# Kernel tuning notes

Measured on AMD Instinct MI355X. Metric: run time of the kernel, lower is better.

## Reference

```python
import jax, jax.numpy as jnp
import numpy as np

HID = 1024
N_HEADS = 16
HEAD_DIM = HID // N_HEADS  # 64
SCALE = float(np.sqrt(HEAD_DIM))  # 8.0
# dba_l1 constants from the source
SCALING = float(np.sqrt(0.72676)) * SCALE
CENTER = SCALE ** 2 * 1.12838


def setup_inputs() -> dict:
    key = jax.random.key(0)
    kq, kk, kv = jax.random.split(key, 3)
    B, LQ, LK = 4, 256, 2048
    return {
        "attention_q": jax.random.normal(kq, (B, LQ, HID), dtype=jnp.float32),
        "attention_k": jax.random.normal(kk, (B, LK, HID), dtype=jnp.float32),
        "attention_v": jax.random.normal(kv, (B, LK, HID), dtype=jnp.float32),
        "attn_diag": jnp.ones((N_HEADS, 1, HEAD_DIM), dtype=jnp.float32),
    }


def _dba_l1_logits(Q, K, attn_diag):
    # Q: [B,H,Lq,D], K: [B,H,Lk,D], attn_diag: [H,1,D]
    # Scan over query positions (mirrors the original per-query loop) to avoid
    # materializing the [B,H,Lq,Lk,D] diff tensor.
    qs = jnp.moveaxis(Q, 2, 0)  # [Lq,B,H,D]

    def step(carry, qi):
        # qi: [B,H,D] -> dist: [B,H,Lk]
        dist = jnp.sum(attn_diag * jnp.abs(K - qi[:, :, None, :]), axis=-1)
        # (dist - CENTER) / (-SCALING) == (CENTER - dist) / SCALING
        return carry, (CENTER - dist) / SCALING

    _, logits = jax.lax.scan(step, None, qs)  # [Lq,B,H,Lk]
    return jnp.moveaxis(logits, 0, 2)  # [B,H,Lq,Lk]


def reference(attention_q, attention_k, attention_v, attn_diag):
    B, Lq, _ = attention_q.shape
    Lk = attention_k.shape[1]
    # split heads: [B,L,hid] -> [B,H,L,D]
    Q = attention_q.reshape(B, Lq, N_HEADS, HEAD_DIM).transpose(0, 2, 1, 3)
    K = attention_k.reshape(B, Lk, N_HEADS, HEAD_DIM).transpose(0, 2, 1, 3)
    V = attention_v.reshape(B, Lk, N_HEADS, HEAD_DIM).transpose(0, 2, 1, 3)

    attn_logits = _dba_l1_logits(Q, K, attn_diag)  # [B,H,Lq,Lk]
    attention = jax.nn.softmax(attn_logits, axis=-1)
    x = jnp.einsum("bhqk,bhkd->bhqd", attention, V)  # [B,H,Lq,D]
    output = x.transpose(0, 2, 1, 3).reshape(B, Lq, HID)
    return output, attention
```

## Files before the change

kernel.cpp:

```cpp
#include <hip/hip_runtime.h>
#include <stdint.h>

typedef _Float16 half_t;
typedef _Float16 h8_t __attribute__((ext_vector_type(8)));
typedef _Float16 h4_t __attribute__((ext_vector_type(4)));
typedef float f4 __attribute__((ext_vector_type(4)));
typedef unsigned int u4v __attribute__((ext_vector_type(4)));

#define NB 4
#define NH 16
#define HD 64
#define LQ 256
#define LK 2048
#define HIDN 1024

#define KF 0.21153832f
#define QS 2048.0f
#define PSTR 2056

__device__ __forceinline__ uint32_t sad16(uint32_t a, uint32_t b, uint32_t c) {
  uint32_t d;
  asm("v_sad_u16 %0, %1, %2, %3" : "=v"(d) : "v"(a), "v"(b), "v"(c));
  return d;
}
__device__ __forceinline__ uint32_t umin32(uint32_t a, uint32_t b) { return a < b ? a : b; }

__device__ __forceinline__ uint32_t quant2(float x0, float x1, float w0, float w1) {
  float f0 = fmaf(x0, w0, 32768.5f);
  float f1 = fmaf(x1, w1, 32768.5f);
  uint32_t u0 = (uint32_t)fminf(fmaxf(f0, 0.f), 65535.f);
  uint32_t u1 = (uint32_t)fminf(fmaxf(f1, 0.f), 65535.f);
  return u0 | (u1 << 16);
}

__global__ __launch_bounds__(256) void k_prep4(const float* __restrict__ Kin,
                                               const float* __restrict__ Vin,
                                               const float* __restrict__ diag,
                                               uint32_t* __restrict__ Ktq,
                                               half_t* __restrict__ Vfrag) {
  int bid = blockIdx.x;
  int isV = bid >= NB * NH * 32;
  int id = isV ? bid - NB * NH * 32 : bid;
  int kb = id & 31, bh = id >> 5, b = bh >> 4, h = bh & 15;
  int t = threadIdx.x;
  __shared__ float ls[64][65];
  {
    const float* base = isV ? Vin : Kin;
    int d = t & 63, kr = t >> 6;
    const float* src = base + (size_t)(b * LK + kb * 64 + kr) * HIDN + h * HD + d;
#pragma unroll
    for (int i = 0; i < 16; ++i) ls[kr + 4 * i][d] = src[(size_t)(4 * i) * HIDN];
  }
  __syncthreads();
  if (!isV) {
    int k = t & 63, g = t >> 6;
    uint32_t* dst = Ktq + ((size_t)bh * 32 + g * 8) * LK + kb * 64 + k;
#pragma unroll
    for (int i = 0; i < 8; ++i) {
      int d2 = g * 8 + i;
      float w0 = diag[h * HD + 2 * d2] * QS;
      float w1 = diag[h * HD + 2 * d2 + 1] * QS;
      dst[(size_t)i * LK] = quant2(ls[k][2 * d2], ls[k][2 * d2 + 1], w0, w1);
    }
  } else {
    half_t* dst = Vfrag + (size_t)bh * (HD * LK) + (size_t)kb * 4096;
#pragma unroll
    for (int i = 0; i < 2; ++i) {
      int s = t * 2 + i;
      int kcl = s >> 8, nt = (s >> 6) & 3, ln = s & 63;
      int kr = kcl * 32 + (ln >> 4) * 8;
      int n = nt * 16 + (ln & 15);
      h8_t v;
#pragma unroll
      for (int j = 0; j < 8; ++j) v[j] = (half_t)ls[kr + j][n];
      *(h8_t*)(dst + (size_t)s * 8) = v;
    }
  }
}

__global__ __launch_bounds__(512, 4) void k_fused(const float* __restrict__ Qin,
                                                  const uint32_t* __restrict__ Ktq,
                                                  const float* __restrict__ diag,
                                                  const half_t* __restrict__ Vfrag,
                                                  float* __restrict__ attn,
                                                  float* __restrict__ Xout) {
  int bid = blockIdx.x;
  int bh = bid & 63, qt = bid >> 6;
  int b = bh >> 4, h = bh & 15;
  int q0 = qt * 8, t = threadIdx.x;
  int lane = t & 63, wid = t >> 6;
  int m = lane & 15, quad = lane >> 4;

  __shared__ uint32_t Qsp[8][32];
  __shared__ __align__(16) float redf[8][8];
  __shared__ __align__(16) uint32_t redu[8][8];
  __shared__ __align__(16) char ShBuf[8 * PSTR * 2];
  half_t* Pst = (half_t*)ShBuf;
  float* Cred = (float*)ShBuf;

  if (t < 256) {
    int q = t >> 5, d2 = t & 31;
    const float* qr = Qin + (size_t)(b * LQ + q0 + q) * HIDN + h * HD;
    float2 f = ((const float2*)qr)[d2];
    float2 w = ((const float2*)(diag + h * HD))[d2];
    Qsp[q][d2] = quant2(f.x, f.y, w.x * QS, w.y * QS);
  }
  __syncthreads();

  uint32_t acc[8][4];
#pragma unroll
  for (int q = 0; q < 8; ++q)
#pragma unroll
    for (int k = 0; k < 4; ++k) acc[q][k] = 0u;

  const uint32_t* kp = Ktq + (size_t)bh * 32 * LK + t * 4;
#pragma unroll 2
  for (int g = 0; g < 16; ++g) {
    u4v ka = *(const u4v*)kp;
    u4v kb = *(const u4v*)(kp + LK);
    kp += 2 * LK;
#pragma unroll
    for (int q = 0; q < 8; ++q) {
      uint2 qd = *(const uint2*)&Qsp[q][2 * g];
#pragma unroll
      for (int k = 0; k < 4; ++k)
        acc[q][k] = sad16(kb[k], qd.y, sad16(ka[k], qd.x, acc[q][k]));
    }
  }

  uint32_t mrow[8];
#pragma unroll
  for (int q = 0; q < 8; ++q) {
    uint32_t mn = umin32(umin32(acc[q][0], acc[q][1]), umin32(acc[q][2], acc[q][3]));
#pragma unroll
    for (int off = 32; off; off >>= 1)
      mn = umin32(mn, (uint32_t)__shfl_xor((int)mn, off, 64));
    mrow[q] = mn;
  }
  if (lane == 0) {
#pragma unroll
    for (int q = 0; q < 8; ++q) redu[q][wid] = mrow[q];
  }
  __syncthreads();
#pragma unroll
  for (int q = 0; q < 8; ++q) {
    u4v a = *(const u4v*)&redu[q][0];
    u4v c = *(const u4v*)&redu[q][4];
    mrow[q] = umin32(umin32(umin32(a[0], a[1]), umin32(a[2], a[3])),
                     umin32(umin32(c[0], c[1]), umin32(c[2], c[3])));
  }

  const float KFQ = KF / QS;
  float pv[8][4];
  float rsum[8];
#pragma unroll
  for (int q = 0; q < 8; ++q) {
    float s = 0.f;
#pragma unroll
    for (int k = 0; k < 4; ++k) {
      float p = exp2f((float)((int)mrow[q] - (int)acc[q][k]) * KFQ);
      pv[q][k] = p;
      s += p;
    }
#pragma unroll
    for (int off = 32; off; off >>= 1) s += __shfl_xor(s, off, 64);
    rsum[q] = s;
  }
  if (lane == 0) {
#pragma unroll
    for (int q = 0; q < 8; ++q) redf[q][wid] = rsum[q];
  }
  __syncthreads();
#pragma unroll
  for (int q = 0; q < 8; ++q) {
    f4 a = *(const f4*)&redf[q][0];
    f4 c = *(const f4*)&redf[q][4];
    rsum[q] = ((a[0] + a[1]) + (a[2] + a[3])) + ((c[0] + c[1]) + (c[2] + c[3]));
  }

#pragma unroll
  for (int q = 0; q < 8; ++q) {
    float inv = 1.0f / rsum[q];
    f4 p;
    h4_t hp;
#pragma unroll
    for (int i = 0; i < 4; ++i) {
      p[i] = pv[q][i] * inv;
      hp[i] = (half_t)p[i];
    }
    size_t row = (size_t)(bh * LQ + q0 + q) * LK + t * 4;
    __builtin_nontemporal_store(p, (f4*)(attn + row));
    *(h4_t*)(Pst + q * PSTR + t * 4) = hp;
  }

  f4 cfr[4];
#pragma unroll
  for (int nt = 0; nt < 4; ++nt) cfr[nt] = (f4){0.f, 0.f, 0.f, 0.f};
  const half_t* vf = Vfrag + (size_t)bh * (HD * LK);
#pragma unroll 2
  for (int c = 0; c < 8; ++c) {
    int kc = wid * 8 + c;
    h8_t af = *(const h8_t*)(Pst + (m & 7) * PSTR + kc * 32 + quad * 8);
#pragma unroll
    for (int nt = 0; nt < 4; ++nt) {
      h8_t bf = *(const h8_t*)(vf + (size_t)((kc * 4 + nt) * 64 + lane) * 8);
      cfr[nt] = __builtin_amdgcn_mfma_f32_16x16x32_f16(af, bf, cfr[nt], 0, 0, 0);
    }
  }

  __syncthreads();
  if (quad < 2) {
#pragma unroll
    for (int nt = 0; nt < 4; ++nt)
#pragma unroll
      for (int r = 0; r < 4; ++r)
        Cred[((wid * 8 + quad * 4 + r) * 64) + nt * 16 + m] = cfr[nt][r];
  }
  __syncthreads();

  {
    int q = t >> 6, d = t & 63;
    float s = 0.f;
#pragma unroll
    for (int w = 0; w < 8; ++w) s += Cred[((w * 8 + q) * 64) + d];
    __builtin_nontemporal_store(s, Xout + (size_t)(b * LQ + q0 + q) * HIDN + h * HD + d);
  }
}

__global__ __launch_bounds__(256, 2) void k_attn_slow(const float* __restrict__ Qin,
                                                      const float* __restrict__ Kin,
                                                      const float* __restrict__ diag,
                                                      float* __restrict__ attn) {
  int bid = blockIdx.x;
  int qt = bid & 15, bh = bid >> 4;
  int b = bh >> 4, h = bh & 15;
  int q0 = qt * 16, t = threadIdx.x;
  __shared__ float Qs[16][64];
  __shared__ float Dg[64];
  __shared__ float red[4][16];
  {
    int q = t >> 4;
    const f4* src = (const f4*)(Qin + (size_t)(b * LQ + q0 + q) * HIDN + h * HD);
    ((f4*)Qs[q])[t & 15] = src[t & 15];
  }
  if (t < 64) Dg[t] = diag[h * HD + t];
  __syncthreads();
  float acc[16][8];
#pragma unroll
  for (int q = 0; q < 16; ++q)
#pragma unroll
    for (int j = 0; j < 8; ++j) acc[q][j] = 0.f;
  const float* kfp = Kin + (size_t)(b * LK + t * 8) * HIDN + h * HD;
  for (int d = 0; d < 64; ++d) {
    float dgd = Dg[d];
    float kd[8];
#pragma unroll
    for (int j = 0; j < 8; ++j) kd[j] = kfp[(size_t)j * HIDN + d];
#pragma unroll
    for (int j = 0; j < 8; ++j) {
      float kv = kd[j];
#pragma unroll
      for (int q = 0; q < 16; ++q)
        acc[q][j] = fmaf(dgd, fabsf(kv - Qs[q][d]), acc[q][j]);
    }
  }
  int lane = t & 63, wid = t >> 6;
  float mrow[16];
#pragma unroll
  for (int q = 0; q < 16; ++q) {
    float mm = acc[q][0];
#pragma unroll
    for (int j = 1; j < 8; ++j) mm = fminf(mm, acc[q][j]);
#pragma unroll
    for (int off = 32; off; off >>= 1) mm = fminf(mm, __shfl_xor(mm, off, 64));
    mrow[q] = mm;
  }
  if (lane == 0)
#pragma unroll
    for (int q = 0; q < 16; ++q) red[wid][q] = mrow[q];
  __syncthreads();
#pragma unroll
  for (int q = 0; q < 16; ++q)
    mrow[q] = fminf(fminf(red[0][q], red[1][q]), fminf(red[2][q], red[3][q]));
  __syncthreads();
  float rsum[16];
#pragma unroll
  for (int q = 0; q < 16; ++q) {
    float s = 0.f;
#pragma unroll
    for (int j = 0; j < 8; ++j) {
      float p = exp2f((mrow[q] - acc[q][j]) * KF);
      acc[q][j] = p;
      s += p;
    }
#pragma unroll
    for (int off = 32; off; off >>= 1) s += __shfl_xor(s, off, 64);
    rsum[q] = s;
  }
  if (lane == 0)
#pragma unroll
    for (int q = 0; q < 16; ++q) red[wid][q] = rsum[q];
  __syncthreads();
#pragma unroll
  for (int q = 0; q < 16; ++q)
    rsum[q] = (red[0][q] + red[1][q]) + (red[2][q] + red[3][q]);
#pragma unroll
  for (int q = 0; q < 16; ++q) {
    float inv = 1.0f / rsum[q];
    f4 p0, p1;
#pragma unroll
    for (int i = 0; i < 4; ++i) { p0[i] = acc[q][i] * inv; p1[i] = acc[q][4 + i] * inv; }
    float* op = attn + ((size_t)(bh * LQ + q0 + q)) * LK + t * 8;
    ((f4*)op)[0] = p0;
    ((f4*)op)[1] = p1;
  }
}

__global__ __launch_bounds__(256) void k_pv_old(const float* __restrict__ P,
                                                const float* __restrict__ Vin,
                                                float* __restrict__ Xout) {
  int bid = blockIdx.x;
  int qt = bid & 3, bh = bid >> 2;
  int b = bh >> 4, h = bh & 15;
  int q0 = qt * 64;
  int t = threadIdx.x, lane = t & 63, wid = t >> 6;
  int m = lane & 15, quad = lane >> 4;
  __shared__ half_t Vts[64 * 256];
  f4 cfr[4];
#pragma unroll
  for (int nt = 0; nt < 4; ++nt) cfr[nt] = (f4){0.f, 0.f, 0.f, 0.f};
  int qrow = q0 + wid * 16 + m;
  const float* pbase = P + ((size_t)(bh * LQ + qrow)) * LK + quad * 8;
  for (int kb = 0; kb < 8; ++kb) {
    {
      int d = wid * 16 + (lane & 15);
      int kg = lane >> 4;
      const float* vp = Vin + (size_t)(b * LK + kb * 256) * HIDN + h * HD + d;
#pragma unroll
      for (int i = 0; i < 32; ++i) {
        int kl = i * 8 + kg * 2;
        float v0 = vp[(size_t)kl * HIDN];
        float v1 = vp[(size_t)(kl + 1) * HIDN];
        int addr = d * 256 + ((((kl >> 3) ^ (d & 7)) << 3) | (kl & 7));
        Vts[addr] = (half_t)v0;
        Vts[addr + 1] = (half_t)v1;
      }
    }
    __syncthreads();
#pragma unroll
    for (int ks = 0; ks < 8; ++ks) {
      const float* pp = pbase + kb * 256 + ks * 32;
      f4 a0 = ((const f4*)pp)[0];
      f4 a1 = ((const f4*)pp)[1];
      h8_t af;
#pragma unroll
      for (int i = 0; i < 4; ++i) { af[i] = (half_t)a0[i]; af[4 + i] = (half_t)a1[i]; }
      int koff = ks * 32 + quad * 8;
#pragma unroll
      for (int nt = 0; nt < 4; ++nt) {
        int n = nt * 16 + m;
        int vaddr = n * 256 + ((((koff >> 3) ^ (n & 7)) << 3));
        h8_t bf = *(const h8_t*)&Vts[vaddr];
        cfr[nt] = __builtin_amdgcn_mfma_f32_16x16x32_f16(af, bf, cfr[nt], 0, 0, 0);
      }
    }
    __syncthreads();
  }
#pragma unroll
  for (int nt = 0; nt < 4; ++nt)
#pragma unroll
    for (int r = 0; r < 4; ++r) {
      int row = quad * 4 + r;
      int q = q0 + wid * 16 + row;
      Xout[(size_t)(b * LQ + q) * HIDN + h * HD + nt * 16 + m] = cfr[nt][r];
    }
}

extern "C" void kernel_launch(void* const* d_in, const int* in_sizes, int n_in,
                              void* d_out, int out_size, void* d_ws, size_t ws_size,
                              hipStream_t stream) {
  const float* Q = (const float*)d_in[0];
  const float* K = (const float*)d_in[1];
  const float* V = (const float*)d_in[2];
  const float* dg = (const float*)d_in[3];
  float* out = (float*)d_out;
  float* attn = out + (size_t)NB * LQ * HIDN;

  size_t ktB = (size_t)NB * NH * 32 * LK * 4;
  size_t vfB = (size_t)NB * NH * HD * LK * 2;
  char* wsb = (char*)d_ws;
  uint32_t* Ktq = (uint32_t*)wsb;
  half_t* Vfrag = (half_t*)(wsb + ktB);

  if (ws_size >= ktB + vfB) {
    k_prep4<<<NB * NH * 32 * 2, 256, 0, stream>>>(K, V, dg, Ktq, Vfrag);
    k_fused<<<NB * NH * 32, 512, 0, stream>>>(Q, Ktq, dg, Vfrag, attn, out);
  } else {
    k_attn_slow<<<NB * NH * 16, 256, 0, stream>>>(Q, K, dg, attn);
    k_pv_old<<<NB * NH * 4, 256, 0, stream>>>(attn, V, out);
  }
}
```

Measured before the change: 259.4 us.

## Split fused attention into SAD-softmax kernel and separate fp16 PV MFMA kernel

Replaces the single fused logits+softmax+PV kernel with two kernels when workspace allows. The first computes L1-distance logits with packed SAD, applies softmax, and writes both the fp32 attention and an fp16 copy to workspace. The second runs the PV product with MFMA from that fp16 copy. This aims to free the first kernel from PV register and LDS pressure, at the cost of an extra global write and read of the fp16 probability matrix and one more launch.

New measurement: 294.9 us. 1.14x slower.

```diff
diff --git a/kernel.cpp b/kernel.cpp
--- a/kernel.cpp
+++ b/kernel.cpp
@@ -78,6 +78,144 @@
   }
 }
 
+__global__ __launch_bounds__(512, 4) void k_sad(const float* __restrict__ Qin,
+                                                const uint32_t* __restrict__ Ktq,
+                                                const float* __restrict__ diag,
+                                                float* __restrict__ attn,
+                                                half_t* __restrict__ P16) {
+  int bid = blockIdx.x;
+  int bh = bid & 63, qt = bid >> 6;
+  int b = bh >> 4, h = bh & 15;
+  int q0 = qt * 8, t = threadIdx.x;
+  int lane = t & 63, wid = t >> 6;
+
+  __shared__ uint32_t Qsp[8][32];
+  __shared__ __align__(16) float redf[8][8];
+  __shared__ __align__(16) uint32_t redu[8][8];
+
+  if (t < 256) {
+    int q = t >> 5, d2 = t & 31;
+    const float* qr = Qin + (size_t)(b * LQ + q0 + q) * HIDN + h * HD;
+    float2 f = ((const float2*)qr)[d2];
+    float2 w = ((const float2*)(diag + h * HD))[d2];
+    Qsp[q][d2] = quant2(f.x, f.y, w.x * QS, w.y * QS);
+  }
+  __syncthreads();
+
+  uint32_t acc[8][4];
+#pragma unroll
+  for (int q = 0; q < 8; ++q)
+#pragma unroll
+    for (int k = 0; k < 4; ++k) acc[q][k] = 0u;
+
+  const uint32_t* kp = Ktq + (size_t)bh * 32 * LK + t * 4;
+#pragma unroll 2
+  for (int g = 0; g < 16; ++g) {
+    u4v ka = *(const u4v*)kp;
+    u4v kb = *(const u4v*)(kp + LK);
+    kp += 2 * LK;
+#pragma unroll
+    for (int q = 0; q < 8; ++q) {
+      uint2 qd = *(const uint2*)&Qsp[q][2 * g];
+#pragma unroll
+      for (int k = 0; k < 4; ++k)
+        acc[q][k] = sad16(kb[k], qd.y, sad16(ka[k], qd.x, acc[q][k]));
+    }
+  }
+
+  uint32_t mrow[8];
+#pragma unroll
+  for (int q = 0; q < 8; ++q) {
+    uint32_t mn = umin32(umin32(acc[q][0], acc[q][1]), umin32(acc[q][2], acc[q][3]));
+#pragma unroll
+    for (int off = 32; off; off >>= 1)
+      mn = umin32(mn, (uint32_t)__shfl_xor((int)mn, off, 64));
+    mrow[q] = mn;
+  }
+  if (lane == 0) {
+#pragma unroll
+    for (int q = 0; q < 8; ++q) redu[q][wid] = mrow[q];
+  }
+  __syncthreads();
+#pragma unroll
+  for (int q = 0; q < 8; ++q) {
+    u4v a = *(const u4v*)&redu[q][0];
+    u4v c = *(const u4v*)&redu[q][4];
+    mrow[q] = umin32(umin32(umin32(a[0], a[1]), umin32(a[2], a[3])),
+                     umin32(umin32(c[0], c[1]), umin32(c[2], c[3])));
+  }
+
+  const float KFQ = KF / QS;
+  float pv[8][4];
+  float rsum[8];
+#pragma unroll
+  for (int q = 0; q < 8; ++q) {
+    float s = 0.f;
+#pragma unroll
+    for (int k = 0; k < 4; ++k) {
+      float p = exp2f((float)((int)mrow[q] - (int)acc[q][k]) * KFQ);
+      pv[q][k] = p;
+      s += p;
+    }
+#pragma unroll
+    for (int off = 32; off; off >>= 1) s += __shfl_xor(s, off, 64);
+    rsum[q] = s;
+  }
+  if (lane == 0) {
+#pragma unroll
+    for (int q = 0; q < 8; ++q) redf[q][wid] = rsum[q];
+  }
+  __syncthreads();
+#pragma unroll
+  for (int q = 0; q < 8; ++q) {
+    f4 a = *(const f4*)&redf[q][0];
+    f4 c = *(const f4*)&redf[q][4];
+    rsum[q] = ((a[0] + a[1]) + (a[2] + a[3])) + ((c[0] + c[1]) + (c[2] + c[3]));
+  }
+
+#pragma unroll
+  for (int q = 0; q < 8; ++q) {
+    float inv = 1.0f / rsum[q];
+    f4 p;
+    h4_t hp;
+#pragma unroll
+    for (int i = 0; i < 4; ++i) {
+      p[i] = pv[q][i] * inv;
+      hp[i] = (half_t)p[i];
+    }
+    size_t row = (size_t)(bh * LQ + q0 + q) * LK + t * 4;
+    __builtin_nontemporal_store(p, (f4*)(attn + row));
+    *(h4_t*)(P16 + row) = hp;
+  }
+}
+
+__global__ __launch_bounds__(256) void k_pv(const half_t* __restrict__ P16,
+                                            const half_t* __restrict__ Vfrag,
+                                            float* __restrict__ Xout) {
+  int bid = blockIdx.x;
+  int bh = bid & 63, qt = bid >> 6;
+  int b = bh >> 4, h = bh & 15;
+  int t = threadIdx.x, lane = t & 63, w = t >> 6;
+  int m = lane & 15, quad = lane >> 4;
+
+  const half_t* pb = P16 + ((size_t)(bh * LQ + qt * 16 + m)) * LK + quad * 8;
+  const half_t* vb = Vfrag + (size_t)bh * (HD * LK) + ((size_t)w * 64 + lane) * 8;
+
+  f4 c = {0.f, 0.f, 0.f, 0.f};
+#pragma unroll 4
+  for (int kc = 0; kc < 64; ++kc) {
+    h8_t af = *(const h8_t*)(pb + kc * 32);
+    h8_t bf = *(const h8_t*)(vb + (size_t)kc * 2048);
+    c = __builtin_amdgcn_mfma_f32_16x16x32_f16(af, bf, c, 0, 0, 0);
+  }
+#pragma unroll
+  for (int r = 0; r < 4; ++r) {
+    int q = qt * 16 + quad * 4 + r;
+    __builtin_nontemporal_store(
+        c[r], Xout + (size_t)(b * LQ + q) * HIDN + h * HD + w * 16 + m);
+  }
+}
+
 __global__ __launch_bounds__(512, 4) void k_fused(const float* __restrict__ Qin,
                                                   const uint32_t* __restrict__ Ktq,
                                                   const float* __restrict__ diag,
@@ -388,11 +526,17 @@
 
   size_t ktB = (size_t)NB * NH * 32 * LK * 4;
   size_t vfB = (size_t)NB * NH * HD * LK * 2;
+  size_t p16B = (size_t)NB * NH * LQ * LK * 2;
   char* wsb = (char*)d_ws;
   uint32_t* Ktq = (uint32_t*)wsb;
   half_t* Vfrag = (half_t*)(wsb + ktB);
-
-  if (ws_size >= ktB + vfB) {
+  half_t* P16 = (half_t*)(wsb + ktB + vfB);
+
+  if (ws_size >= ktB + vfB + p16B) {
+    k_prep4<<<NB * NH * 32 * 2, 256, 0, stream>>>(K, V, dg, Ktq, Vfrag);
+    k_sad<<<NB * NH * 32, 512, 0, stream>>>(Q, Ktq, dg, attn, P16);
+    k_pv<<<NB * NH * 16, 256, 0, stream>>>(P16, Vfrag, out);
+  } else if (ws_size >= ktB + vfB) {
     k_prep4<<<NB * NH * 32 * 2, 256, 0, stream>>>(K, V, dg, Ktq, Vfrag);
     k_fused<<<NB * NH * 32, 512, 0, stream>>>(Q, Ktq, dg, Vfrag, attn, out);
   } else {
```
